# Optimization experiments

Measured on AMD Instinct MI355X. Metric: run time of the kernel, lower is better.

The kernel has to match this reference:

```python
import jax, jax.numpy as jnp
import numpy as np

C = 256
R = 16
CR = C // R  # 16

def setup_inputs() -> dict:
    key = jax.random.key(0)
    k1, k2, k3 = jax.random.split(key, 3)
    x = jax.random.normal(k1, (16, C, 128, 128), dtype=jnp.float32)
    # 1x1 conv weights expressed as channel matmuls
    w1 = jax.random.normal(k2, (CR, C), dtype=jnp.float32) * (1.0 / np.sqrt(C))
    b1 = jnp.zeros((CR,), dtype=jnp.float32)
    w2 = jax.random.normal(k3, (C, CR), dtype=jnp.float32) * (1.0 / np.sqrt(CR))
    b2 = jnp.zeros((C,), dtype=jnp.float32)
    return {"x": x, "w1": w1, "b1": b1, "w2": w2, "b2": b2}

def reference(x, w1, b1, w2, b2):
    # global average pool over H,W -> [B, C]
    y = jnp.mean(x, axis=(2, 3))
    # 1x1 conv MLP: [B,C] @ [C,CR]^T -> relu -> [B,CR] @ [CR,C]^T -> sigmoid
    y = jax.nn.relu(jnp.einsum('bc,rc->br', y, w1) + b1)
    y = jax.nn.sigmoid(jnp.einsum('br,cr->bc', y, w2) + b2)
    # channel gating broadcast back onto x
    return x * y[:, :, None, None]
```

## Files before the change

kernel.cpp:

```cpp
#include <hip/hip_runtime.h>
#include <hip/hip_bf16.h>
#include <math.h>

#define PLANE 16384
#define PLANE4 4096
#define NPLANES 4096
#define NB 16
#define NC 256
#define NR 16

typedef float vfloat4 __attribute__((ext_vector_type(4)));

__global__ __launch_bounds__(256) void pool_kernel(const float* __restrict__ x,
                                                   float* __restrict__ mean) {
    const size_t base = (size_t)blockIdx.x * PLANE;
    const vfloat4* xp = (const vfloat4*)(x + base);
    const int tid = threadIdx.x;
    float s = 0.f;
    #pragma unroll
    for (int j = 0; j < 16; ++j) {
        vfloat4 v = xp[tid + j * 256];
        s += (v.x + v.y) + (v.z + v.w);
    }
    #pragma unroll
    for (int o = 32; o > 0; o >>= 1) s += __shfl_down(s, o, 64);
    __shared__ float wsum[4];
    if ((tid & 63) == 0) wsum[tid >> 6] = s;
    __syncthreads();
    if (tid == 0) {
        float t = (wsum[0] + wsum[1]) + (wsum[2] + wsum[3]);
        mean[blockIdx.x] = t * (1.0f / (float)PLANE);
    }
}

__global__ __launch_bounds__(256) void scale_kernel(const float* __restrict__ x,
                                                    const float* __restrict__ mean,
                                                    const float* __restrict__ w1,
                                                    const float* __restrict__ b1,
                                                    const float* __restrict__ w2,
                                                    const float* __restrict__ b2,
                                                    float* __restrict__ out) {
    const int plane = NPLANES - 1 - blockIdx.x;
    const int b = plane >> 8;
    const int c = plane & (NC - 1);
    const int tid = threadIdx.x;
    const int wave = tid >> 6;
    const int lane = tid & 63;

    __shared__ float hsh[NR];
    __shared__ float gsh;

    {
        const vfloat4 yv = ((const vfloat4*)(mean + b * NC))[lane];
        #pragma unroll
        for (int k = 0; k < 4; ++k) {
            const int r = wave * 4 + k;
            const vfloat4 wv = ((const vfloat4*)(w1 + r * NC))[lane];
            float p = yv.x * wv.x + yv.y * wv.y + yv.z * wv.z + yv.w * wv.w;
            #pragma unroll
            for (int o = 32; o > 0; o >>= 1) p += __shfl_down(p, o, 64);
            if (lane == 0) hsh[r] = fmaxf(p + b1[r], 0.f);
        }
    }
    __syncthreads();
    if (tid == 0) {
        float a = b2[c];
        #pragma unroll
        for (int r = 0; r < NR; ++r) a += hsh[r] * w2[c * NR + r];
        gsh = 1.0f / (1.0f + expf(-a));
    }
    __syncthreads();
    const float g = gsh;

    const size_t base = (size_t)plane * PLANE;
    const vfloat4* xp = (const vfloat4*)(x + base);
    vfloat4* op = (vfloat4*)(out + base);
    #pragma unroll
    for (int j = 0; j < 16; ++j) {
        vfloat4 v = xp[tid + j * 256];
        v.x *= g; v.y *= g; v.z *= g; v.w *= g;
        __builtin_nontemporal_store(v, op + tid + j * 256);
    }
}

extern "C" void kernel_launch(void* const* d_in, const int* in_sizes, int n_in,
                              void* d_out, int out_size, void* d_ws, size_t ws_size,
                              hipStream_t stream) {
    const float* x  = (const float*)d_in[0];
    const float* w1 = (const float*)d_in[1];
    const float* b1 = (const float*)d_in[2];
    const float* w2 = (const float*)d_in[3];
    const float* b2 = (const float*)d_in[4];
    float* out = (float*)d_out;

    float* mean = (float*)d_ws;

    pool_kernel<<<NPLANES, 256, 0, stream>>>(x, mean);
    scale_kernel<<<NPLANES, 256, 0, stream>>>(x, mean, w1, b1, w2, b2, out);
}
```

Before: 482.6 us.

## Split gate MLP into its own kernel and batch loads in pool/scale

Moves the per-plane recomputation of the squeeze-excite MLP out of the scale kernel into a small 16-block gate kernel that writes all gates once. The scale kernel then only reads one gate value and streams the plane. Both memory kernels now issue loads in batches of eight before consuming them, and use launch bounds with occupancy hints. The plane order is reversed in groups of eight to reuse cache from the pool pass. This adds an extra kernel launch and a serial dependency.

```diff
diff --git a/kernel.cpp b/kernel.cpp
--- a/kernel.cpp
+++ b/kernel.cpp
@@ -1,9 +1,7 @@
 #include <hip/hip_runtime.h>
-#include <hip/hip_bf16.h>
 #include <math.h>
 
 #define PLANE 16384
-#define PLANE4 4096
 #define NPLANES 4096
 #define NB 16
 #define NC 256
@@ -11,16 +9,19 @@
 
 typedef float vfloat4 __attribute__((ext_vector_type(4)));
 
-__global__ __launch_bounds__(256) void pool_kernel(const float* __restrict__ x,
-                                                   float* __restrict__ mean) {
+__global__ __launch_bounds__(256, 8) void pool_kernel(const float* __restrict__ x,
+                                                      float* __restrict__ mean) {
     const size_t base = (size_t)blockIdx.x * PLANE;
     const vfloat4* xp = (const vfloat4*)(x + base);
     const int tid = threadIdx.x;
     float s = 0.f;
     #pragma unroll
-    for (int j = 0; j < 16; ++j) {
-        vfloat4 v = xp[tid + j * 256];
-        s += (v.x + v.y) + (v.z + v.w);
+    for (int h = 0; h < 2; ++h) {
+        vfloat4 v[8];
+        #pragma unroll
+        for (int j = 0; j < 8; ++j) v[j] = xp[tid + (h * 8 + j) * 256];
+        #pragma unroll
+        for (int j = 0; j < 8; ++j) s += (v[j].x + v[j].y) + (v[j].z + v[j].w);
     }
     #pragma unroll
     for (int o = 32; o > 0; o >>= 1) s += __shfl_down(s, o, 64);
@@ -28,28 +29,22 @@
     if ((tid & 63) == 0) wsum[tid >> 6] = s;
     __syncthreads();
     if (tid == 0) {
-        float t = (wsum[0] + wsum[1]) + (wsum[2] + wsum[3]);
-        mean[blockIdx.x] = t * (1.0f / (float)PLANE);
+        mean[blockIdx.x] = ((wsum[0] + wsum[1]) + (wsum[2] + wsum[3])) * (1.0f / (float)PLANE);
     }
 }
 
-__global__ __launch_bounds__(256) void scale_kernel(const float* __restrict__ x,
-                                                    const float* __restrict__ mean,
-                                                    const float* __restrict__ w1,
-                                                    const float* __restrict__ b1,
-                                                    const float* __restrict__ w2,
-                                                    const float* __restrict__ b2,
-                                                    float* __restrict__ out) {
-    const int plane = NPLANES - 1 - blockIdx.x;
-    const int b = plane >> 8;
-    const int c = plane & (NC - 1);
+__global__ __launch_bounds__(256) void gate_kernel(const float* __restrict__ mean,
+                                                   const float* __restrict__ w1,
+                                                   const float* __restrict__ b1,
+                                                   const float* __restrict__ w2,
+                                                   const float* __restrict__ b2,
+                                                   float* __restrict__ gate) {
+    const int b = blockIdx.x;
     const int tid = threadIdx.x;
     const int wave = tid >> 6;
     const int lane = tid & 63;
 
     __shared__ float hsh[NR];
-    __shared__ float gsh;
-
     {
         const vfloat4 yv = ((const vfloat4*)(mean + b * NC))[lane];
         #pragma unroll
@@ -63,23 +58,34 @@
         }
     }
     __syncthreads();
-    if (tid == 0) {
-        float a = b2[c];
-        #pragma unroll
-        for (int r = 0; r < NR; ++r) a += hsh[r] * w2[c * NR + r];
-        gsh = 1.0f / (1.0f + expf(-a));
-    }
-    __syncthreads();
-    const float g = gsh;
+    const int c = tid;
+    float a = b2[c];
+    #pragma unroll
+    for (int r = 0; r < NR; ++r) a += hsh[r] * w2[c * NR + r];
+    gate[b * NC + c] = 1.0f / (1.0f + expf(-a));
+}
 
+__global__ __launch_bounds__(256, 8) void scale_kernel(const float* __restrict__ x,
+                                                       const float* __restrict__ gate,
+                                                       float* __restrict__ out) {
+    const int i = blockIdx.x;
+    const int plane = (4088 - (i & ~7)) + (i & 7);
+    const float g = gate[plane];
     const size_t base = (size_t)plane * PLANE;
     const vfloat4* xp = (const vfloat4*)(x + base);
     vfloat4* op = (vfloat4*)(out + base);
+    const int tid = threadIdx.x;
     #pragma unroll
-    for (int j = 0; j < 16; ++j) {
-        vfloat4 v = xp[tid + j * 256];
-        v.x *= g; v.y *= g; v.z *= g; v.w *= g;
-        __builtin_nontemporal_store(v, op + tid + j * 256);
+    for (int h = 0; h < 2; ++h) {
+        vfloat4 v[8];
+        #pragma unroll
+        for (int j = 0; j < 8; ++j) v[j] = xp[tid + (h * 8 + j) * 256];
+        #pragma unroll
+        for (int j = 0; j < 8; ++j) {
+            vfloat4 w = v[j];
+            w.x *= g; w.y *= g; w.z *= g; w.w *= g;
+            __builtin_nontemporal_store(w, op + tid + (h * 8 + j) * 256);
+        }
     }
 }
 
@@ -94,7 +100,9 @@
     float* out = (float*)d_out;
 
     float* mean = (float*)d_ws;
+    float* gate = mean + NPLANES;
 
     pool_kernel<<<NPLANES, 256, 0, stream>>>(x, mean);
-    scale_kernel<<<NPLANES, 256, 0, stream>>>(x, mean, w1, b1, w2, b2, out);
+    gate_kernel<<<NB, 256, 0, stream>>>(mean, w1, b1, w2, b2, gate);
+    scale_kernel<<<NPLANES, 256, 0, stream>>>(x, gate, out);
 }
```

Measured after the change: 483.2 us. About the same (+0.1%).
